# Kernel tuning notes

Hardware: AMD Instinct MI355X
Metric: run time of the kernel (lower is better)

The kernel has to match this reference:

```python
import jax, jax.numpy as jnp
import numpy as np

B, N, CIN, DIM = 4, 16384, 32, 256
NPOINT, NNEIGH = 2048, 16
BN_EPS = 1e-5


def setup_inputs() -> dict:
    key = jax.random.key(0)
    ks = jax.random.split(key, 6)
    return {
        "xyz": jax.random.normal(ks[0], (B, N, 3), jnp.float32),
        "points": jax.random.normal(ks[1], (B, N, CIN), jnp.float32),
        "fc1_w": jax.random.normal(ks[2], (CIN, DIM), jnp.float32) * 0.05,
        "fc1_b": jnp.zeros((DIM,), jnp.float32),
        "conv1_w": jax.random.normal(ks[3], (DIM, DIM), jnp.float32) * 0.05,
        "conv1_b": jnp.zeros((DIM,), jnp.float32),
        "conv2_w": jax.random.normal(ks[4], (DIM, DIM), jnp.float32) * 0.05,
        "conv2_b": jnp.zeros((DIM,), jnp.float32),
        "bn1_g": jnp.ones((DIM,), jnp.float32),
        "bn1_b": jnp.zeros((DIM,), jnp.float32),
        "bn2_g": jnp.ones((DIM,), jnp.float32),
        "bn2_b": jnp.zeros((DIM,), jnp.float32),
        "bn_g": jnp.ones((DIM,), jnp.float32),
        "bn_b": jnp.zeros((DIM,), jnp.float32),
        "npoint": NPOINT,
        "nneigh": NNEIGH,
    }


def _gather(p, i):
    # p: [B, N, ...], i: [B, ...int] -> per-batch fancy index
    return jax.vmap(lambda a, b: a[b])(p, i)


def _batchnorm(x, g, b):
    # x: [B, S, C]; torch BatchNorm1d training-mode forward over (B, S)
    m = x.mean((0, 1), keepdims=True)
    v = x.var((0, 1), keepdims=True)  # biased variance, as torch uses in forward
    return (x - m) * jax.lax.rsqrt(v + BN_EPS) * g + b


def _fps(xyz, npoint):
    # furthest point sampling, seeded at index 0 (pointnet2_utils convention)
    Bn, Nn, _ = xyz.shape
    dist0 = jnp.full((Bn, Nn), jnp.inf, xyz.dtype)
    far0 = jnp.zeros((Bn,), jnp.int32)

    def step(carry, _):
        dist, far = carry
        cent = _gather(xyz, far)  # [B, 3]
        d = jnp.sum((xyz - cent[:, None, :]) ** 2, axis=-1)  # [B, N]
        dist = jnp.minimum(dist, d)
        nxt = jnp.argmax(dist, axis=-1).astype(jnp.int32)
        return (dist, nxt), far

    _, idx = jax.lax.scan(step, (dist0, far0), None, length=npoint)
    return idx.T  # [B, npoint]


def _square_distance(a, b):
    # a: [B, S, 3], b: [B, N, 3] -> [B, S, N]
    return (jnp.sum(a * a, -1)[..., :, None]
            + jnp.sum(b * b, -1)[..., None, :]
            - 2.0 * jnp.einsum('bsc,bnc->bsn', a, b))


def reference(xyz, points, fc1_w, fc1_b, conv1_w, conv1_b, conv2_w, conv2_b,
              bn1_g, bn1_b, bn2_g, bn2_b, bn_g, bn_b, npoint, nneigh):
    fps_idx = _fps(jax.lax.stop_gradient(xyz), npoint)          # [B, S]
    new_xyz = _gather(xyz, fps_idx)                              # [B, S, 3]

    h = points @ fc1_w + fc1_b                                   # [B, N, D]
    points_ori = _gather(h, fps_idx)                             # [B, S, D]

    t = jax.nn.relu(_batchnorm(h @ conv1_w.T + conv1_b, bn1_g, bn1_b))
    h = h + jax.nn.relu(_batchnorm(t @ conv2_w.T + conv2_b, bn2_g, bn2_b))

    d = _square_distance(jax.lax.stop_gradient(new_xyz), jax.lax.stop_gradient(xyz))
    _, idx = jax.lax.top_k(-d, nneigh)                           # [B, S, K] smallest dists
    grouped = _gather(h, idx)                                    # [B, S, K, D]
    new_points = points_ori + grouped.max(axis=2)                # [B, S, D]
    new_points = _batchnorm(new_points, bn_g, bn_b)
    return new_xyz, new_points
```

## Files before the change

### kernel.cpp

```cpp
#include <hip/hip_runtime.h>
#include <math.h>

#define Bn   4
#define Nn   16384
#define CINn 32
#define DIMn 256
#define Sn   2048
#define KNEI 16
#define BNEPS 1e-5f
#define MROWS (Bn * Nn)
#define SROWS (Bn * Sn)

#define UMAX_DPP(v, ctl, rmask)                                               \
    {                                                                         \
        unsigned _o = (unsigned)__builtin_amdgcn_update_dpp(                  \
            0, (int)(v), (ctl), (rmask), 0xf, true);                          \
        (v) = ((v) > _o) ? (v) : _o;                                          \
    }
#define WAVE_UMAX64(v)                                                        \
    UMAX_DPP(v, 0x111, 0xf) UMAX_DPP(v, 0x112, 0xf) UMAX_DPP(v, 0x114, 0xf)  \
    UMAX_DPP(v, 0x118, 0xf) UMAX_DPP(v, 0x142, 0xa) UMAX_DPP(v, 0x143, 0xc)
#define U64MAX_DPP16(khi, klo, ctl)                                           \
    {                                                                         \
        unsigned _lo2 = (unsigned)__builtin_amdgcn_update_dpp(                \
            0, (int)(klo), (ctl), 0xf, 0xf, true);                            \
        unsigned _hi2 = (unsigned)__builtin_amdgcn_update_dpp(                \
            0, (int)(khi), (ctl), 0xf, 0xf, true);                            \
        const bool _g = (_hi2 > (khi)) || (_hi2 == (khi) && _lo2 > (klo));    \
        (khi) = _g ? _hi2 : (khi);                                            \
        (klo) = _g ? _lo2 : (klo);                                            \
    }

__global__ __launch_bounds__(1024, 1) void fps_kernel(const float* __restrict__ xyz,
                                                      int* __restrict__ fidx,
                                                      float* __restrict__ newxyz)
{
#pragma clang fp contract(off)
    __shared__ float sx[1024 * 20];
    __shared__ unsigned long long s_wk[2][16];
    const int b = blockIdx.x;
    const int t = threadIdx.x;
    const int w = t >> 6;
    const int lane = t & 63;
    const float* __restrict__ px = xyz + (size_t)b * Nn * 3;

    float y[16], z[16], dist[16];
#pragma unroll
    for (int a = 0; a < 12; ++a) {
        const float4 v = *reinterpret_cast<const float4*>(&px[48 * t + 4 * a]);
        const float e[4] = {v.x, v.y, v.z, v.w};
#pragma unroll
        for (int c = 0; c < 4; ++c) {
            const int flat = 4 * a + c;
            const int j = flat / 3;
            const int comp = flat - 3 * j;
            if (comp == 0) sx[20 * t + j] = e[c];
            else if (comp == 1) y[j] = e[c];
            else z[j] = e[c];
        }
    }
#pragma unroll
    for (int j = 0; j < 16; ++j) {
        dist[j] = __builtin_huge_valf();
        asm volatile("" : "+v"(y[j]));
        asm volatile("" : "+v"(z[j]));
    }
    float cx = px[0], cy = px[1], cz = px[2];
    if (t == 0) {
        fidx[b * Sn] = 0;
        newxyz[(size_t)b * Sn * 3 + 0] = cx;
        newxyz[(size_t)b * Sn * 3 + 1] = cy;
        newxyz[(size_t)b * Sn * 3 + 2] = cz;
    }
    __syncthreads();

    for (int i = 0; i < Sn - 1; ++i) {
        float bd = -1.0f;
#pragma unroll
        for (int a = 0; a < 4; ++a) {
            const float4 q = *reinterpret_cast<const float4*>(&sx[20 * t + 4 * a]);
            const float xv[4] = {q.x, q.y, q.z, q.w};
#pragma unroll
            for (int c = 0; c < 4; ++c) {
                const int j = 4 * a + c;
                const float dx = xv[c] - cx;
                const float dy = y[j] - cy;
                const float dz = z[j] - cz;
                const float d = (dx * dx + dy * dy) + dz * dz;
                const float nd = fminf(dist[j], d);
                dist[j] = nd;
                bd = fmaxf(bd, nd);
            }
        }
        unsigned bn = 0;
#pragma unroll
        for (int j = 15; j >= 0; --j)
            if (dist[j] == bd) bn = 0xFFFFFFFFu - (unsigned)(16 * t + j);
        unsigned bdu = __float_as_uint(bd);
        unsigned m = bdu;
        WAVE_UMAX64(m)
        const unsigned bdw = (unsigned)__builtin_amdgcn_readlane((int)m, 63);
        unsigned q2 = (bdu == bdw) ? bn : 0u;
        WAVE_UMAX64(q2)
        const unsigned bnw = (unsigned)__builtin_amdgcn_readlane((int)q2, 63);
        if (lane == 0)
            s_wk[i & 1][w] = ((unsigned long long)bdw << 32) | bnw;
        __syncthreads();
        const unsigned long long kk =
            (lane < 16) ? s_wk[i & 1][lane] : 0ull;
        unsigned klo = (unsigned)kk;
        unsigned khi = (unsigned)(kk >> 32);
        U64MAX_DPP16(khi, klo, 0x111)
        U64MAX_DPP16(khi, klo, 0x112)
        U64MAX_DPP16(khi, klo, 0x114)
        U64MAX_DPP16(khi, klo, 0x118)
        const unsigned bnf = (unsigned)__builtin_amdgcn_readlane((int)klo, 15);
        const int wu = (int)(0xFFFFFFFFu - bnf);
        cx = px[3 * wu + 0];
        cy = px[3 * wu + 1];
        cz = px[3 * wu + 2];
        if (t == 0) {
            fidx[b * Sn + i + 1] = wu;
            newxyz[(size_t)(b * Sn + i + 1) * 3 + 0] = cx;
            newxyz[(size_t)(b * Sn + i + 1) * 3 + 1] = cy;
            newxyz[(size_t)(b * Sn + i + 1) * 3 + 2] = cz;
        }
    }
}

template <bool BT, bool AFF>
__global__ __launch_bounds__(256) void gemm_k(const float* __restrict__ A,
                                              const float* __restrict__ Bm,
                                              const float* __restrict__ bias,
                                              const float* __restrict__ asc,
                                              const float* __restrict__ ash,
                                              float* __restrict__ C, int K)
{
    __shared__ float As[16][64];
    __shared__ float Bs[16][64];
    const int t = threadIdx.x;
    const int tx = t & 15;
    const int ty = t >> 4;
    const int r0 = blockIdx.x * 64;
    const int c0 = blockIdx.y * 64;
    const int rrA = t >> 2;
    const int kkA = (t & 3) * 4;
    float acc[4][4] = {};
    for (int kc = 0; kc < K; kc += 16) {
        {
            const float4 v = *reinterpret_cast<const float4*>(
                &A[(size_t)(r0 + rrA) * K + kc + kkA]);
            float vv[4] = {v.x, v.y, v.z, v.w};
#pragma unroll
            for (int m = 0; m < 4; ++m) {
                float xv = vv[m];
                if (AFF) {
                    const int k = kc + kkA + m;
                    xv = fmaxf(fmaf(xv, asc[k], ash[k]), 0.0f);
                }
                As[kkA + m][rrA] = xv;
            }
        }
        if (BT) {
            const float4 v = *reinterpret_cast<const float4*>(
                &Bm[(size_t)(c0 + rrA) * K + kc + kkA]);
            Bs[kkA + 0][rrA] = v.x;
            Bs[kkA + 1][rrA] = v.y;
            Bs[kkA + 2][rrA] = v.z;
            Bs[kkA + 3][rrA] = v.w;
        } else {
            const int kk = t >> 4;
            const int cc = (t & 15) * 4;
            const float4 v = *reinterpret_cast<const float4*>(
                &Bm[(size_t)(kc + kk) * DIMn + c0 + cc]);
            *reinterpret_cast<float4*>(&Bs[kk][cc]) = v;
        }
        __syncthreads();
#pragma unroll
        for (int kk = 0; kk < 16; ++kk) {
            const float4 a = *reinterpret_cast<const float4*>(&As[kk][ty * 4]);
            const float4 bv = *reinterpret_cast<const float4*>(&Bs[kk][tx * 4]);
            const float av[4] = {a.x, a.y, a.z, a.w};
            const float bw[4] = {bv.x, bv.y, bv.z, bv.w};
#pragma unroll
            for (int i = 0; i < 4; ++i)
#pragma unroll
                for (int j = 0; j < 4; ++j)
                    acc[i][j] = fmaf(av[i], bw[j], acc[i][j]);
        }
        __syncthreads();
    }
    const int c = c0 + tx * 4;
#pragma unroll
    for (int i = 0; i < 4; ++i) {
        float4 o;
        o.x = acc[i][0] + bias[c + 0];
        o.y = acc[i][1] + bias[c + 1];
        o.z = acc[i][2] + bias[c + 2];
        o.w = acc[i][3] + bias[c + 3];
        *reinterpret_cast<float4*>(&C[(size_t)(r0 + ty * 4 + i) * DIMn + c]) = o;
    }
}

__global__ __launch_bounds__(256) void gather_po_kernel(const float* __restrict__ h0,
                                                        const int* __restrict__ fidx,
                                                        float* __restrict__ pre)
{
    const int bs = blockIdx.x;
    const int b = bs >> 11;
    const int fid = fidx[bs];
    pre[(size_t)bs * DIMn + threadIdx.x] =
        h0[((size_t)b * Nn + fid) * DIMn + threadIdx.x];
}

__global__ __launch_bounds__(256) void stats_partial(const float* __restrict__ X,
                                                     int rowsPerBlk,
                                                     float* __restrict__ ps,
                                                     float* __restrict__ pq)
{
    const int c = threadIdx.x;
    const size_t r0 = (size_t)blockIdx.x * rowsPerBlk;
    float s = 0.0f, q = 0.0f;
    for (int r = 0; r < rowsPerBlk; ++r) {
        const float v = X[(r0 + r) * DIMn + c];
        s += v;
        q = fmaf(v, v, q);
    }
    ps[blockIdx.x * DIMn + c] = s;
    pq[blockIdx.x * DIMn + c] = q;
}

__global__ __launch_bounds__(256) void bn_finalize(const float* __restrict__ ps,
                                                   const float* __restrict__ pq,
                                                   int nblk, float invN,
                                                   const float* __restrict__ g,
                                                   const float* __restrict__ bb,
                                                   float* __restrict__ sc,
                                                   float* __restrict__ sh)
{
    const int c = threadIdx.x;
    float s = 0.0f, q = 0.0f;
    for (int i = 0; i < nblk; ++i) {
        s += ps[i * DIMn + c];
        q += pq[i * DIMn + c];
    }
    const float mean = s * invN;
    const float var = q * invN - mean * mean;
    const float r = 1.0f / sqrtf(var + BNEPS);
    const float scale = g[c] * r;
    sc[c] = scale;
    sh[c] = bb[c] - mean * scale;
}

__global__ __launch_bounds__(256) void residual_kernel(float* __restrict__ h,
                                                       const float* __restrict__ a2,
                                                       const float* __restrict__ sc,
                                                       const float* __restrict__ sh)
{
    const size_t i = (size_t)blockIdx.x * 256 + threadIdx.x;
    const int c4 = (int)(i & 63);
    float4 hv = reinterpret_cast<float4*>(h)[i];
    const float4 av = reinterpret_cast<const float4*>(a2)[i];
    const float4 s4 = reinterpret_cast<const float4*>(sc)[c4];
    const float4 b4 = reinterpret_cast<const float4*>(sh)[c4];
    hv.x += fmaxf(fmaf(av.x, s4.x, b4.x), 0.0f);
    hv.y += fmaxf(fmaf(av.y, s4.y, b4.y), 0.0f);
    hv.z += fmaxf(fmaf(av.z, s4.z, b4.z), 0.0f);
    hv.w += fmaxf(fmaf(av.w, s4.w, b4.w), 0.0f);
    reinterpret_cast<float4*>(h)[i] = hv;
}

__global__ __launch_bounds__(256) void topk_group(const float* __restrict__ xyz,
                                                  const float* __restrict__ newxyz,
                                                  const float* __restrict__ h,
                                                  float* __restrict__ pre)
{
#pragma clang fp contract(off)
    __shared__ unsigned s_key[Nn];
    __shared__ unsigned long long s_wred[4];
    __shared__ unsigned long long s_win;
    __shared__ int s_nidx[KNEI];
    const int bs = blockIdx.x;
    const int b = bs >> 11;
    const int t = threadIdx.x;
    const float* px = xyz + (size_t)b * Nn * 3;
    const float qx = newxyz[bs * 3 + 0];
    const float qy = newxyz[bs * 3 + 1];
    const float qz = newxyz[bs * 3 + 2];
    const float qq = (qx * qx + qy * qy) + qz * qz;
    unsigned long long mkey = ~0ull;
#pragma unroll 4
    for (int u = 0; u < 64; ++u) {
        const int n = t + (u << 8);
        const float bx = px[n * 3 + 0];
        const float by = px[n * 3 + 1];
        const float bz = px[n * 3 + 2];
        const float bb2 = (bx * bx + by * by) + bz * bz;
        const float ab = (qx * bx + qy * by) + qz * bz;
        const float d = (qq + bb2) - 2.0f * ab;
        unsigned u32 = __float_as_uint(d);
        u32 = ((int)u32 < 0) ? ~u32 : (u32 | 0x80000000u);
        s_key[n] = u32;
        const unsigned long long k = ((unsigned long long)u32 << 32) | (unsigned)n;
        mkey = (k < mkey) ? k : mkey;
    }
    __syncthreads();
    for (int r = 0; r < KNEI; ++r) {
        unsigned long long k = mkey;
#pragma unroll
        for (int off = 32; off > 0; off >>= 1) {
            const unsigned long long o = __shfl_xor(k, off);
            k = (o < k) ? o : k;
        }
        if ((t & 63) == 0) s_wred[t >> 6] = k;
        __syncthreads();
        if (t == 0) {
            unsigned long long w = s_wred[0];
            if (s_wred[1] < w) w = s_wred[1];
            if (s_wred[2] < w) w = s_wred[2];
            if (s_wred[3] < w) w = s_wred[3];
            s_win = w;
            s_nidx[r] = (int)(unsigned)(w & 0xFFFFFFFFull);
        }
        __syncthreads();
        const unsigned long long w = s_win;
        if (w == mkey) {
            const int wn = (int)(unsigned)(w & 0xFFFFFFFFull);
            s_key[wn] = 0xFFFFFFFFu;
            mkey = ~0ull;
#pragma unroll 4
            for (int u = 0; u < 64; ++u) {
                const int n = t + (u << 8);
                const unsigned long long kk =
                    ((unsigned long long)s_key[n] << 32) | (unsigned)n;
                mkey = (kk < mkey) ? kk : mkey;
            }
        }
        __syncthreads();
    }
    const float po = pre[(size_t)bs * DIMn + t];
    float m = -__builtin_huge_valf();
#pragma unroll
    for (int r = 0; r < KNEI; ++r) {
        const int n = s_nidx[r];
        m = fmaxf(m, h[((size_t)b * Nn + n) * DIMn + t]);
    }
    pre[(size_t)bs * DIMn + t] = po + m;
}

__global__ __launch_bounds__(256) void apply_bn_kernel(const float* __restrict__ pre,
                                                       const float* __restrict__ sc,
                                                       const float* __restrict__ sh,
                                                       float* __restrict__ out)
{
    const size_t i = (size_t)blockIdx.x * 256 + threadIdx.x;
    const int c4 = (int)(i & 63);
    const float4 v = reinterpret_cast<const float4*>(pre)[i];
    const float4 s4 = reinterpret_cast<const float4*>(sc)[c4];
    const float4 b4 = reinterpret_cast<const float4*>(sh)[c4];
    float4 o;
    o.x = fmaf(v.x, s4.x, b4.x);
    o.y = fmaf(v.y, s4.y, b4.y);
    o.z = fmaf(v.z, s4.z, b4.z);
    o.w = fmaf(v.w, s4.w, b4.w);
    reinterpret_cast<float4*>(out)[i] = o;
}

extern "C" void kernel_launch(void* const* d_in, const int* in_sizes, int n_in,
                              void* d_out, int out_size, void* d_ws, size_t ws_size,
                              hipStream_t stream)
{
    (void)in_sizes; (void)n_in; (void)out_size; (void)ws_size;
    const float* xyz     = (const float*)d_in[0];
    const float* points  = (const float*)d_in[1];
    const float* fc1_w   = (const float*)d_in[2];
    const float* fc1_b   = (const float*)d_in[3];
    const float* conv1_w = (const float*)d_in[4];
    const float* conv1_b = (const float*)d_in[5];
    const float* conv2_w = (const float*)d_in[6];
    const float* conv2_b = (const float*)d_in[7];
    const float* bn1_g   = (const float*)d_in[8];
    const float* bn1_b   = (const float*)d_in[9];
    const float* bn2_g   = (const float*)d_in[10];
    const float* bn2_b   = (const float*)d_in[11];
    const float* bn_g    = (const float*)d_in[12];
    const float* bn_b    = (const float*)d_in[13];

    float* out = (float*)d_out;
    float* newxyz = out;
    float* outpts = out + (size_t)Bn * Sn * 3;

    char* w = (char*)d_ws;
    float* h0   = (float*)(w);
    float* A1   = (float*)(w + (64ull << 20));
    float* A2   = (float*)(w + (128ull << 20));
    float* pre  = (float*)(w + (192ull << 20));
    int*   fidx = (int*)  (w + (200ull << 20));
    float* ps   = (float*)(w + (201ull << 20));
    float* pq   = ps + 256 * 256;
    float* sc1  = pq + 256 * 256;
    float* sh1  = sc1 + 256;
    float* sc2  = sh1 + 256;
    float* sh2  = sc2 + 256;
    float* sc3  = sh2 + 256;
    float* sh3  = sc3 + 256;

    fps_kernel<<<Bn, 1024, 0, stream>>>(xyz, fidx, newxyz);
    gemm_k<false, false><<<dim3(MROWS / 64, DIMn / 64), 256, 0, stream>>>(
        points, fc1_w, fc1_b, nullptr, nullptr, h0, CINn);
    gather_po_kernel<<<SROWS, 256, 0, stream>>>(h0, fidx, pre);
    gemm_k<true, false><<<dim3(MROWS / 64, DIMn / 64), 256, 0, stream>>>(
        h0, conv1_w, conv1_b, nullptr, nullptr, A1, DIMn);
    stats_partial<<<256, 256, 0, stream>>>(A1, MROWS / 256, ps, pq);
    bn_finalize<<<1, 256, 0, stream>>>(ps, pq, 256, 1.0f / MROWS, bn1_g, bn1_b, sc1, sh1);
    gemm_k<true, true><<<dim3(MROWS / 64, DIMn / 64), 256, 0, stream>>>(
        A1, conv2_w, conv2_b, sc1, sh1, A2, DIMn);
    stats_partial<<<256, 256, 0, stream>>>(A2, MROWS / 256, ps, pq);
    bn_finalize<<<1, 256, 0, stream>>>(ps, pq, 256, 1.0f / MROWS, bn2_g, bn2_b, sc2, sh2);
    residual_kernel<<<(MROWS * DIMn / 4) / 256, 256, 0, stream>>>(h0, A2, sc2, sh2);
    topk_group<<<SROWS, 256, 0, stream>>>(xyz, newxyz, h0, pre);
    stats_partial<<<64, 256, 0, stream>>>(pre, SROWS / 64, ps, pq);
    bn_finalize<<<1, 256, 0, stream>>>(ps, pq, 64, 1.0f / SROWS, bn_g, bn_b, sc3, sh3);
    apply_bn_kernel<<<(SROWS * DIMn / 4) / 256, 256, 0, stream>>>(pre, sc3, sh3, outpts);
}
```

Baseline: 4.668 ms.

## Fuse FPS, MLP stages and kNN grouping into one persistent kernel

Merges the sequential FPS kernel with the GEMM, BN-stats, residual and top-k grouping stages into a single persistent launch of 252 blocks. Four blocks run FPS while the other 248 work blocks process the MLP stages behind grid-wide atomic barriers. The kNN grouping then consumes FPS progress through per-batch counters published every 256 points. The aim is to hide the long serial FPS latency behind the dense work and to remove launch overhead. It depends on every block being resident at the same time to avoid deadlock, and it adds spin-wait barrier cost.

```diff
diff --git a/kernel.cpp b/kernel.cpp
--- a/kernel.cpp
+++ b/kernel.cpp
@@ -10,6 +10,14 @@
 #define BNEPS 1e-5f
 #define MROWS (Bn * Nn)
 #define SROWS (Bn * Sn)
+
+#define NWORK 248
+#define NBLK  (NWORK + Bn)
+
+struct FusedSync {
+    unsigned stage[8];
+    unsigned prog[Bn];
+};
 
 #define UMAX_DPP(v, ctl, rmask)                                               \
     {                                                                         \
@@ -31,126 +39,29 @@
         (klo) = _g ? _lo2 : (klo);                                            \
     }
 
-__global__ __launch_bounds__(1024, 1) void fps_kernel(const float* __restrict__ xyz,
-                                                      int* __restrict__ fidx,
-                                                      float* __restrict__ newxyz)
-{
-#pragma clang fp contract(off)
-    __shared__ float sx[1024 * 20];
-    __shared__ unsigned long long s_wk[2][16];
-    const int b = blockIdx.x;
-    const int t = threadIdx.x;
-    const int w = t >> 6;
-    const int lane = t & 63;
-    const float* __restrict__ px = xyz + (size_t)b * Nn * 3;
-
-    float y[16], z[16], dist[16];
-#pragma unroll
-    for (int a = 0; a < 12; ++a) {
-        const float4 v = *reinterpret_cast<const float4*>(&px[48 * t + 4 * a]);
-        const float e[4] = {v.x, v.y, v.z, v.w};
-#pragma unroll
-        for (int c = 0; c < 4; ++c) {
-            const int flat = 4 * a + c;
-            const int j = flat / 3;
-            const int comp = flat - 3 * j;
-            if (comp == 0) sx[20 * t + j] = e[c];
-            else if (comp == 1) y[j] = e[c];
-            else z[j] = e[c];
-        }
-    }
-#pragma unroll
-    for (int j = 0; j < 16; ++j) {
-        dist[j] = __builtin_huge_valf();
-        asm volatile("" : "+v"(y[j]));
-        asm volatile("" : "+v"(z[j]));
-    }
-    float cx = px[0], cy = px[1], cz = px[2];
-    if (t == 0) {
-        fidx[b * Sn] = 0;
-        newxyz[(size_t)b * Sn * 3 + 0] = cx;
-        newxyz[(size_t)b * Sn * 3 + 1] = cy;
-        newxyz[(size_t)b * Sn * 3 + 2] = cz;
-    }
-    __syncthreads();
-
-    for (int i = 0; i < Sn - 1; ++i) {
-        float bd = -1.0f;
-#pragma unroll
-        for (int a = 0; a < 4; ++a) {
-            const float4 q = *reinterpret_cast<const float4*>(&sx[20 * t + 4 * a]);
-            const float xv[4] = {q.x, q.y, q.z, q.w};
-#pragma unroll
-            for (int c = 0; c < 4; ++c) {
-                const int j = 4 * a + c;
-                const float dx = xv[c] - cx;
-                const float dy = y[j] - cy;
-                const float dz = z[j] - cz;
-                const float d = (dx * dx + dy * dy) + dz * dz;
-                const float nd = fminf(dist[j], d);
-                dist[j] = nd;
-                bd = fmaxf(bd, nd);
-            }
-        }
-        unsigned bn = 0;
-#pragma unroll
-        for (int j = 15; j >= 0; --j)
-            if (dist[j] == bd) bn = 0xFFFFFFFFu - (unsigned)(16 * t + j);
-        unsigned bdu = __float_as_uint(bd);
-        unsigned m = bdu;
-        WAVE_UMAX64(m)
-        const unsigned bdw = (unsigned)__builtin_amdgcn_readlane((int)m, 63);
-        unsigned q2 = (bdu == bdw) ? bn : 0u;
-        WAVE_UMAX64(q2)
-        const unsigned bnw = (unsigned)__builtin_amdgcn_readlane((int)q2, 63);
-        if (lane == 0)
-            s_wk[i & 1][w] = ((unsigned long long)bdw << 32) | bnw;
-        __syncthreads();
-        const unsigned long long kk =
-            (lane < 16) ? s_wk[i & 1][lane] : 0ull;
-        unsigned klo = (unsigned)kk;
-        unsigned khi = (unsigned)(kk >> 32);
-        U64MAX_DPP16(khi, klo, 0x111)
-        U64MAX_DPP16(khi, klo, 0x112)
-        U64MAX_DPP16(khi, klo, 0x114)
-        U64MAX_DPP16(khi, klo, 0x118)
-        const unsigned bnf = (unsigned)__builtin_amdgcn_readlane((int)klo, 15);
-        const int wu = (int)(0xFFFFFFFFu - bnf);
-        cx = px[3 * wu + 0];
-        cy = px[3 * wu + 1];
-        cz = px[3 * wu + 2];
-        if (t == 0) {
-            fidx[b * Sn + i + 1] = wu;
-            newxyz[(size_t)(b * Sn + i + 1) * 3 + 0] = cx;
-            newxyz[(size_t)(b * Sn + i + 1) * 3 + 1] = cy;
-            newxyz[(size_t)(b * Sn + i + 1) * 3 + 2] = cz;
-        }
-    }
+__global__ __launch_bounds__(64) void fps_zero_kernel(unsigned* __restrict__ s)
+{
+    if (threadIdx.x < 12) s[threadIdx.x] = 0u;
 }
 
 template <bool BT, bool AFF>
-__global__ __launch_bounds__(256) void gemm_k(const float* __restrict__ A,
-                                              const float* __restrict__ Bm,
-                                              const float* __restrict__ bias,
-                                              const float* __restrict__ asc,
-                                              const float* __restrict__ ash,
-                                              float* __restrict__ C, int K)
-{
-    __shared__ float As[16][64];
-    __shared__ float Bs[16][64];
-    const int t = threadIdx.x;
-    const int tx = t & 15;
-    const int ty = t >> 4;
-    const int r0 = blockIdx.x * 64;
-    const int c0 = blockIdx.y * 64;
-    const int rrA = t >> 2;
-    const int kkA = (t & 3) * 4;
+__device__ void gemm_team(const float* A, const float* Bm, const float* bias,
+                          const float* asc, const float* ash, float* C,
+                          int K, int tile, bool act, float* lAs, float* lBs,
+                          int ts)
+{
+    const int tx = ts & 15;
+    const int ty = ts >> 4;
+    const int r0 = (tile >> 2) * 64;
+    const int c0 = (tile & 3) * 64;
+    const int rrA = ts >> 2;
+    const int kkA = (ts & 3) * 4;
     float acc[4][4] = {};
     for (int kc = 0; kc < K; kc += 16) {
-        {
+        if (act) {
             const float4 v = *reinterpret_cast<const float4*>(
                 &A[(size_t)(r0 + rrA) * K + kc + kkA]);
-            float vv[4] = {v.x, v.y, v.z, v.w};
+            const float vv[4] = {v.x, v.y, v.z, v.w};
 #pragma unroll
             for (int m = 0; m < 4; ++m) {
                 float xv = vv[m];
@@ -158,59 +69,364 @@
                     const int k = kc + kkA + m;
                     xv = fmaxf(fmaf(xv, asc[k], ash[k]), 0.0f);
                 }
-                As[kkA + m][rrA] = xv;
-            }
-        }
-        if (BT) {
-            const float4 v = *reinterpret_cast<const float4*>(
-                &Bm[(size_t)(c0 + rrA) * K + kc + kkA]);
-            Bs[kkA + 0][rrA] = v.x;
-            Bs[kkA + 1][rrA] = v.y;
-            Bs[kkA + 2][rrA] = v.z;
-            Bs[kkA + 3][rrA] = v.w;
-        } else {
-            const int kk = t >> 4;
-            const int cc = (t & 15) * 4;
-            const float4 v = *reinterpret_cast<const float4*>(
-                &Bm[(size_t)(kc + kk) * DIMn + c0 + cc]);
-            *reinterpret_cast<float4*>(&Bs[kk][cc]) = v;
+                lAs[(kkA + m) * 64 + rrA] = xv;
+            }
+            if (BT) {
+                const float4 u = *reinterpret_cast<const float4*>(
+                    &Bm[(size_t)(c0 + rrA) * K + kc + kkA]);
+                lBs[(kkA + 0) * 64 + rrA] = u.x;
+                lBs[(kkA + 1) * 64 + rrA] = u.y;
+                lBs[(kkA + 2) * 64 + rrA] = u.z;
+                lBs[(kkA + 3) * 64 + rrA] = u.w;
+            } else {
+                const int kk = ts >> 4;
+                const int cc = (ts & 15) * 4;
+                const float4 u = *reinterpret_cast<const float4*>(
+                    &Bm[(size_t)(kc + kk) * DIMn + c0 + cc]);
+                *reinterpret_cast<float4*>(&lBs[kk * 64 + cc]) = u;
+            }
         }
         __syncthreads();
-#pragma unroll
-        for (int kk = 0; kk < 16; ++kk) {
-            const float4 a = *reinterpret_cast<const float4*>(&As[kk][ty * 4]);
-            const float4 bv = *reinterpret_cast<const float4*>(&Bs[kk][tx * 4]);
-            const float av[4] = {a.x, a.y, a.z, a.w};
-            const float bw[4] = {bv.x, bv.y, bv.z, bv.w};
-#pragma unroll
-            for (int i = 0; i < 4; ++i)
-#pragma unroll
-                for (int j = 0; j < 4; ++j)
-                    acc[i][j] = fmaf(av[i], bw[j], acc[i][j]);
+        if (act) {
+#pragma unroll
+            for (int kk = 0; kk < 16; ++kk) {
+                const float4 a = *reinterpret_cast<const float4*>(&lAs[kk * 64 + ty * 4]);
+                const float4 bv = *reinterpret_cast<const float4*>(&lBs[kk * 64 + tx * 4]);
+                const float av[4] = {a.x, a.y, a.z, a.w};
+                const float bw[4] = {bv.x, bv.y, bv.z, bv.w};
+#pragma unroll
+                for (int i = 0; i < 4; ++i)
+#pragma unroll
+                    for (int j = 0; j < 4; ++j)
+                        acc[i][j] = fmaf(av[i], bw[j], acc[i][j]);
+            }
         }
         __syncthreads();
     }
-    const int c = c0 + tx * 4;
-#pragma unroll
-    for (int i = 0; i < 4; ++i) {
-        float4 o;
-        o.x = acc[i][0] + bias[c + 0];
-        o.y = acc[i][1] + bias[c + 1];
-        o.z = acc[i][2] + bias[c + 2];
-        o.w = acc[i][3] + bias[c + 3];
-        *reinterpret_cast<float4*>(&C[(size_t)(r0 + ty * 4 + i) * DIMn + c]) = o;
-    }
-}
-
-__global__ __launch_bounds__(256) void gather_po_kernel(const float* __restrict__ h0,
-                                                        const int* __restrict__ fidx,
-                                                        float* __restrict__ pre)
-{
-    const int bs = blockIdx.x;
-    const int b = bs >> 11;
-    const int fid = fidx[bs];
-    pre[(size_t)bs * DIMn + threadIdx.x] =
-        h0[((size_t)b * Nn + fid) * DIMn + threadIdx.x];
+    if (act) {
+        const int c = c0 + tx * 4;
+#pragma unroll
+        for (int i = 0; i < 4; ++i) {
+            float4 o;
+            o.x = acc[i][0] + bias[c + 0];
+            o.y = acc[i][1] + bias[c + 1];
+            o.z = acc[i][2] + bias[c + 2];
+            o.w = acc[i][3] + bias[c + 3];
+            *reinterpret_cast<float4*>(&C[(size_t)(r0 + ty * 4 + i) * DIMn + c]) = o;
+        }
+    }
+}
+
+__device__ inline void stage_sync(unsigned* ctr, int t)
+{
+    __syncthreads();
+    if (t == 0) {
+        __hip_atomic_fetch_add(ctr, 1u, __ATOMIC_RELEASE, __HIP_MEMORY_SCOPE_AGENT);
+        while (__hip_atomic_load(ctr, __ATOMIC_ACQUIRE, __HIP_MEMORY_SCOPE_AGENT)
+               < (unsigned)NWORK)
+            __builtin_amdgcn_s_sleep(2);
+    }
+    __syncthreads();
+}
+
+__global__ __launch_bounds__(1024, 1) void fused_kernel(
+    const float* __restrict__ xyz, const float* __restrict__ points,
+    const float* __restrict__ fc1_w, const float* __restrict__ fc1_b,
+    const float* __restrict__ conv1_w, const float* __restrict__ conv1_b,
+    const float* __restrict__ conv2_w, const float* __restrict__ conv2_b,
+    const float* __restrict__ bn1_g, const float* __restrict__ bn1_b,
+    const float* __restrict__ bn2_g, const float* __restrict__ bn2_b,
+    float* __restrict__ h0, float* __restrict__ A1, float* __restrict__ A2,
+    float* __restrict__ pre, int* __restrict__ fidx,
+    float* __restrict__ ps, float* __restrict__ pq, float* __restrict__ scv,
+    float* __restrict__ newxyz, FusedSync* sync)
+{
+    __shared__ char smem[81920];
+    __shared__ unsigned long long s_aux[33];
+    __shared__ int s_nidx[KNEI];
+    const int t = threadIdx.x;
+
+    if (blockIdx.x < Bn) {
+#pragma clang fp contract(off)
+        float* sx = reinterpret_cast<float*>(smem);
+        unsigned long long (*s_wk)[16] =
+            reinterpret_cast<unsigned long long (*)[16]>(s_aux);
+        const int b = blockIdx.x;
+        const int w = t >> 6;
+        const int lane = t & 63;
+        const float* __restrict__ px = xyz + (size_t)b * Nn * 3;
+        float y[16], z[16], dist[16];
+#pragma unroll
+        for (int a = 0; a < 12; ++a) {
+            const float4 v = *reinterpret_cast<const float4*>(&px[48 * t + 4 * a]);
+            const float e[4] = {v.x, v.y, v.z, v.w};
+#pragma unroll
+            for (int c = 0; c < 4; ++c) {
+                const int flat = 4 * a + c;
+                const int j = flat / 3;
+                const int comp = flat - 3 * j;
+                if (comp == 0) sx[20 * t + j] = e[c];
+                else if (comp == 1) y[j] = e[c];
+                else z[j] = e[c];
+            }
+        }
+#pragma unroll
+        for (int j = 0; j < 16; ++j) {
+            dist[j] = __builtin_huge_valf();
+            asm volatile("" : "+v"(y[j]));
+            asm volatile("" : "+v"(z[j]));
+        }
+        float cx = px[0], cy = px[1], cz = px[2];
+        if (t == 0) {
+            fidx[b * Sn] = 0;
+            newxyz[(size_t)b * Sn * 3 + 0] = cx;
+            newxyz[(size_t)b * Sn * 3 + 1] = cy;
+            newxyz[(size_t)b * Sn * 3 + 2] = cz;
+        }
+        __syncthreads();
+        for (int i = 0; i < Sn - 1; ++i) {
+            float bd = -1.0f;
+#pragma unroll
+            for (int a = 0; a < 4; ++a) {
+                const float4 q = *reinterpret_cast<const float4*>(&sx[20 * t + 4 * a]);
+                const float xv[4] = {q.x, q.y, q.z, q.w};
+#pragma unroll
+                for (int c = 0; c < 4; ++c) {
+                    const int j = 4 * a + c;
+                    const float dx = xv[c] - cx;
+                    const float dy = y[j] - cy;
+                    const float dz = z[j] - cz;
+                    const float d = (dx * dx + dy * dy) + dz * dz;
+                    const float nd = fminf(dist[j], d);
+                    dist[j] = nd;
+                    bd = fmaxf(bd, nd);
+                }
+            }
+            unsigned bn = 0;
+#pragma unroll
+            for (int j = 15; j >= 0; --j)
+                if (dist[j] == bd) bn = 0xFFFFFFFFu - (unsigned)(16 * t + j);
+            unsigned bdu = __float_as_uint(bd);
+            unsigned m = bdu;
+            WAVE_UMAX64(m)
+            const unsigned bdw = (unsigned)__builtin_amdgcn_readlane((int)m, 63);
+            unsigned q2 = (bdu == bdw) ? bn : 0u;
+            WAVE_UMAX64(q2)
+            const unsigned bnw = (unsigned)__builtin_amdgcn_readlane((int)q2, 63);
+            if (lane == 0)
+                s_wk[i & 1][w] = ((unsigned long long)bdw << 32) | bnw;
+            __syncthreads();
+            const unsigned long long kk = (lane < 16) ? s_wk[i & 1][lane] : 0ull;
+            unsigned klo = (unsigned)kk;
+            unsigned khi = (unsigned)(kk >> 32);
+            U64MAX_DPP16(khi, klo, 0x111)
+            U64MAX_DPP16(khi, klo, 0x112)
+            U64MAX_DPP16(khi, klo, 0x114)
+            U64MAX_DPP16(khi, klo, 0x118)
+            const unsigned bnf = (unsigned)__builtin_amdgcn_readlane((int)klo, 15);
+            const int wu = (int)(0xFFFFFFFFu - bnf);
+            cx = px[3 * wu + 0];
+            cy = px[3 * wu + 1];
+            cz = px[3 * wu + 2];
+            if (t == 0) {
+                fidx[b * Sn + i + 1] = wu;
+                newxyz[(size_t)(b * Sn + i + 1) * 3 + 0] = cx;
+                newxyz[(size_t)(b * Sn + i + 1) * 3 + 1] = cy;
+                newxyz[(size_t)(b * Sn + i + 1) * 3 + 2] = cz;
+                if (((i + 2) & 255) == 0)
+                    __hip_atomic_store(&sync->prog[b], (unsigned)(i + 2),
+                                       __ATOMIC_RELEASE, __HIP_MEMORY_SCOPE_AGENT);
+            }
+        }
+        return;
+    }
+
+    const int wid = blockIdx.x - Bn;
+    const int team = t >> 8;
+    const int ts = t & 255;
+    float* lAs = reinterpret_cast<float*>(smem) + team * 2048;
+    float* lBs = lAs + 1024;
+    float* sc1 = scv, *sh1 = scv + 256, *sc2 = scv + 512, *sh2 = scv + 768;
+
+    for (int it = 0; it < 5; ++it) {
+        const int tile = it * (NWORK * 4) + wid * 4 + team;
+        gemm_team<false, false>(points, fc1_w, fc1_b, nullptr, nullptr, h0,
+                                CINn, tile, tile < 4096, lAs, lBs, ts);
+    }
+    stage_sync(&sync->stage[0], t);
+    for (int it = 0; it < 5; ++it) {
+        const int tile = it * (NWORK * 4) + wid * 4 + team;
+        gemm_team<true, false>(h0, conv1_w, conv1_b, nullptr, nullptr, A1,
+                               DIMn, tile, tile < 4096, lAs, lBs, ts);
+    }
+    stage_sync(&sync->stage[1], t);
+    for (int sb = wid; sb < 256; sb += NWORK) {
+        if (t < DIMn) {
+            float s = 0.0f, q = 0.0f;
+            const size_t r0 = (size_t)sb * 256;
+            for (int r = 0; r < 256; ++r) {
+                const float v = A1[(r0 + r) * DIMn + t];
+                s += v;
+                q = fmaf(v, v, q);
+            }
+            ps[sb * DIMn + t] = s;
+            pq[sb * DIMn + t] = q;
+        }
+    }
+    stage_sync(&sync->stage[2], t);
+    if (wid == 0 && t < DIMn) {
+        float s = 0.0f, q = 0.0f;
+        for (int i = 0; i < 256; ++i) { s += ps[i * DIMn + t]; q += pq[i * DIMn + t]; }
+        const float invN = 1.0f / MROWS;
+        const float mean = s * invN;
+        const float var = q * invN - mean * mean;
+        const float r = 1.0f / sqrtf(var + BNEPS);
+        const float scale = bn1_g[t] * r;
+        sc1[t] = scale;
+        sh1[t] = bn1_b[t] - mean * scale;
+    }
+    stage_sync(&sync->stage[3], t);
+    for (int it = 0; it < 5; ++it) {
+        const int tile = it * (NWORK * 4) + wid * 4 + team;
+        gemm_team<true, true>(A1, conv2_w, conv2_b, sc1, sh1, A2,
+                              DIMn, tile, tile < 4096, lAs, lBs, ts);
+    }
+    stage_sync(&sync->stage[4], t);
+    for (int sb = wid; sb < 256; sb += NWORK) {
+        if (t < DIMn) {
+            float s = 0.0f, q = 0.0f;
+            const size_t r0 = (size_t)sb * 256;
+            for (int r = 0; r < 256; ++r) {
+                const float v = A2[(r0 + r) * DIMn + t];
+                s += v;
+                q = fmaf(v, v, q);
+            }
+            ps[sb * DIMn + t] = s;
+            pq[sb * DIMn + t] = q;
+        }
+    }
+    stage_sync(&sync->stage[5], t);
+    if (wid == 0 && t < DIMn) {
+        float s = 0.0f, q = 0.0f;
+        for (int i = 0; i < 256; ++i) { s += ps[i * DIMn + t]; q += pq[i * DIMn + t]; }
+        const float invN = 1.0f / MROWS;
+        const float mean = s * invN;
+        const float var = q * invN - mean * mean;
+        const float r = 1.0f / sqrtf(var + BNEPS);
+        const float scale = bn2_g[t] * r;
+        sc2[t] = scale;
+        sh2[t] = bn2_b[t] - mean * scale;
+    }
+    stage_sync(&sync->stage[6], t);
+    for (size_t idx = (size_t)wid * 1024 + t; idx < (size_t)MROWS * DIMn / 4;
+         idx += (size_t)NWORK * 1024) {
+        const int c4 = (int)(idx & 63);
+        const float4 hv = reinterpret_cast<const float4*>(h0)[idx];
+        float4 av = reinterpret_cast<float4*>(A2)[idx];
+        const float4 s4 = reinterpret_cast<const float4*>(sc2)[c4];
+        const float4 b4 = reinterpret_cast<const float4*>(sh2)[c4];
+        av.x = hv.x + fmaxf(fmaf(av.x, s4.x, b4.x), 0.0f);
+        av.y = hv.y + fmaxf(fmaf(av.y, s4.y, b4.y), 0.0f);
+        av.z = hv.z + fmaxf(fmaf(av.z, s4.z, b4.z), 0.0f);
+        av.w = hv.w + fmaxf(fmaf(av.w, s4.w, b4.w), 0.0f);
+        reinterpret_cast<float4*>(A2)[idx] = av;
+    }
+    stage_sync(&sync->stage[7], t);
+
+    {
+#pragma clang fp contract(off)
+        unsigned* s_key = reinterpret_cast<unsigned*>(smem);
+        const int b = wid & 3;
+        const int w = t >> 6;
+        const int lane = t & 63;
+        const float* px = xyz + (size_t)b * Nn * 3;
+        unsigned cprog = 0;
+        for (int q = wid; q < SROWS; q += NWORK) {
+            const int s = q >> 2;
+            if (t == 0 && cprog < (unsigned)(s + 1)) {
+                unsigned p;
+                do {
+                    p = __hip_atomic_load(&sync->prog[b], __ATOMIC_ACQUIRE,
+                                          __HIP_MEMORY_SCOPE_AGENT);
+                    if (p < (unsigned)(s + 1)) __builtin_amdgcn_s_sleep(8);
+                } while (p < (unsigned)(s + 1));
+                cprog = p;
+            }
+            __syncthreads();
+            const int bs = b * Sn + s;
+            const float qx = newxyz[(size_t)bs * 3 + 0];
+            const float qy = newxyz[(size_t)bs * 3 + 1];
+            const float qz = newxyz[(size_t)bs * 3 + 2];
+            const float qq = (qx * qx + qy * qy) + qz * qz;
+            unsigned long long mkey = ~0ull;
+#pragma unroll 4
+            for (int u = 0; u < 16; ++u) {
+                const int n = t + (u << 10);
+                const float bx = px[n * 3 + 0];
+                const float by = px[n * 3 + 1];
+                const float bz = px[n * 3 + 2];
+                const float bb2 = (bx * bx + by * by) + bz * bz;
+                const float ab = (qx * bx + qy * by) + qz * bz;
+                const float d = (qq + bb2) - 2.0f * ab;
+                unsigned u32 = __float_as_uint(d);
+                u32 = ((int)u32 < 0) ? ~u32 : (u32 | 0x80000000u);
+                s_key[n] = u32;
+                const unsigned long long k =
+                    ((unsigned long long)u32 << 32) | (unsigned)n;
+                mkey = (k < mkey) ? k : mkey;
+            }
+            __syncthreads();
+            for (int r = 0; r < KNEI; ++r) {
+                unsigned long long k = mkey;
+#pragma unroll
+                for (int off = 32; off > 0; off >>= 1) {
+                    const unsigned long long o = __shfl_xor(k, off);
+                    k = (o < k) ? o : k;
+                }
+                if (lane == 0) s_aux[w] = k;
+                __syncthreads();
+                if (w == 0) {
+                    unsigned long long kk = (lane < 16) ? s_aux[lane] : ~0ull;
+#pragma unroll
+                    for (int off = 8; off > 0; off >>= 1) {
+                        const unsigned long long o = __shfl_xor(kk, off);
+                        kk = (o < kk) ? o : kk;
+                    }
+                    if (lane == 0) {
+                        s_aux[32] = kk;
+                        s_nidx[r] = (int)(unsigned)(kk & 0xFFFFFFFFull);
+                    }
+                }
+                __syncthreads();
+                const unsigned long long wk = s_aux[32];
+                if (wk == mkey) {
+                    const int wn = (int)(unsigned)(wk & 0xFFFFFFFFull);
+                    s_key[wn] = 0xFFFFFFFFu;
+                    mkey = ~0ull;
+#pragma unroll 4
+                    for (int u = 0; u < 16; ++u) {
+                        const int n = t + (u << 10);
+                        const unsigned long long kk2 =
+                            ((unsigned long long)s_key[n] << 32) | (unsigned)n;
+                        mkey = (kk2 < mkey) ? kk2 : mkey;
+                    }
+                }
+            }
+            __syncthreads();
+            if (t < DIMn) {
+                const int fid = fidx[bs];
+                const float po = h0[((size_t)b * Nn + fid) * DIMn + t];
+                float m = -__builtin_huge_valf();
+#pragma unroll
+                for (int r = 0; r < KNEI; ++r) {
+                    const int n = s_nidx[r];
+                    m = fmaxf(m, A2[((size_t)b * Nn + n) * DIMn + t]);
+                }
+                pre[(size_t)bs * DIMn + t] = po + m;
+            }
+            __syncthreads();
+        }
+    }
 }
 
 __global__ __launch_bounds__(256) void stats_partial(const float* __restrict__ X,
@@ -250,102 +466,6 @@
     const float scale = g[c] * r;
     sc[c] = scale;
     sh[c] = bb[c] - mean * scale;
-}
-
-__global__ __launch_bounds__(256) void residual_kernel(float* __restrict__ h,
-                                                       const float* __restrict__ a2,
-                                                       const float* __restrict__ sc,
-                                                       const float* __restrict__ sh)
-{
-    const size_t i = (size_t)blockIdx.x * 256 + threadIdx.x;
-    const int c4 = (int)(i & 63);
-    float4 hv = reinterpret_cast<float4*>(h)[i];
-    const float4 av = reinterpret_cast<const float4*>(a2)[i];
-    const float4 s4 = reinterpret_cast<const float4*>(sc)[c4];
-    const float4 b4 = reinterpret_cast<const float4*>(sh)[c4];
-    hv.x += fmaxf(fmaf(av.x, s4.x, b4.x), 0.0f);
-    hv.y += fmaxf(fmaf(av.y, s4.y, b4.y), 0.0f);
-    hv.z += fmaxf(fmaf(av.z, s4.z, b4.z), 0.0f);
-    hv.w += fmaxf(fmaf(av.w, s4.w, b4.w), 0.0f);
-    reinterpret_cast<float4*>(h)[i] = hv;
-}
-
-__global__ __launch_bounds__(256) void topk_group(const float* __restrict__ xyz,
-                                                  const float* __restrict__ newxyz,
-                                                  const float* __restrict__ h,
-                                                  float* __restrict__ pre)
-{
-#pragma clang fp contract(off)
-    __shared__ unsigned s_key[Nn];
-    __shared__ unsigned long long s_wred[4];
-    __shared__ unsigned long long s_win;
-    __shared__ int s_nidx[KNEI];
-    const int bs = blockIdx.x;
-    const int b = bs >> 11;
-    const int t = threadIdx.x;
-    const float* px = xyz + (size_t)b * Nn * 3;
-    const float qx = newxyz[bs * 3 + 0];
-    const float qy = newxyz[bs * 3 + 1];
-    const float qz = newxyz[bs * 3 + 2];
-    const float qq = (qx * qx + qy * qy) + qz * qz;
-    unsigned long long mkey = ~0ull;
-#pragma unroll 4
-    for (int u = 0; u < 64; ++u) {
-        const int n = t + (u << 8);
-        const float bx = px[n * 3 + 0];
-        const float by = px[n * 3 + 1];
-        const float bz = px[n * 3 + 2];
-        const float bb2 = (bx * bx + by * by) + bz * bz;
-        const float ab = (qx * bx + qy * by) + qz * bz;
-        const float d = (qq + bb2) - 2.0f * ab;
-        unsigned u32 = __float_as_uint(d);
-        u32 = ((int)u32 < 0) ? ~u32 : (u32 | 0x80000000u);
-        s_key[n] = u32;
-        const unsigned long long k = ((unsigned long long)u32 << 32) | (unsigned)n;
-        mkey = (k < mkey) ? k : mkey;
-    }
-    __syncthreads();
-    for (int r = 0; r < KNEI; ++r) {
-        unsigned long long k = mkey;
-#pragma unroll
-        for (int off = 32; off > 0; off >>= 1) {
-            const unsigned long long o = __shfl_xor(k, off);
-            k = (o < k) ? o : k;
-        }
-        if ((t & 63) == 0) s_wred[t >> 6] = k;
-        __syncthreads();
-        if (t == 0) {
-            unsigned long long w = s_wred[0];
-            if (s_wred[1] < w) w = s_wred[1];
-            if (s_wred[2] < w) w = s_wred[2];
-            if (s_wred[3] < w) w = s_wred[3];
-            s_win = w;
-            s_nidx[r] = (int)(unsigned)(w & 0xFFFFFFFFull);
-        }
-        __syncthreads();
-        const unsigned long long w = s_win;
-        if (w == mkey) {
-            const int wn = (int)(unsigned)(w & 0xFFFFFFFFull);
-            s_key[wn] = 0xFFFFFFFFu;
-            mkey = ~0ull;
-#pragma unroll 4
-            for (int u = 0; u < 64; ++u) {
-                const int n = t + (u << 8);
-                const unsigned long long kk =
-                    ((unsigned long long)s_key[n] << 32) | (unsigned)n;
-                mkey = (kk < mkey) ? kk : mkey;
-            }
-        }
-        __syncthreads();
-    }
-    const float po = pre[(size_t)bs * DIMn + t];
-    float m = -__builtin_huge_valf();
-#pragma unroll
-    for (int r = 0; r < KNEI; ++r) {
-        const int n = s_nidx[r];
-        m = fmaxf(m, h[((size_t)b * Nn + n) * DIMn + t]);
-    }
-    pre[(size_t)bs * DIMn + t] = po + m;
 }
 
 __global__ __launch_bounds__(256) void apply_bn_kernel(const float* __restrict__ pre,
@@ -398,27 +518,16 @@
     int*   fidx = (int*)  (w + (200ull << 20));
     float* ps   = (float*)(w + (201ull << 20));
     float* pq   = ps + 256 * 256;
-    float* sc1  = pq + 256 * 256;
-    float* sh1  = sc1 + 256;
-    float* sc2  = sh1 + 256;
-    float* sh2  = sc2 + 256;
-    float* sc3  = sh2 + 256;
+    float* scv  = pq + 256 * 256;
+    float* sc3  = scv + 1024;
     float* sh3  = sc3 + 256;
-
-    fps_kernel<<<Bn, 1024, 0, stream>>>(xyz, fidx, newxyz);
-    gemm_k<false, false><<<dim3(MROWS / 64, DIMn / 64), 256, 0, stream>>>(
-        points, fc1_w, fc1_b, nullptr, nullptr, h0, CINn);
-    gather_po_kernel<<<SROWS, 256, 0, stream>>>(h0, fidx, pre);
-    gemm_k<true, false><<<dim3(MROWS / 64, DIMn / 64), 256, 0, stream>>>(
-        h0, conv1_w, conv1_b, nullptr, nullptr, A1, DIMn);
-    stats_partial<<<256, 256, 0, stream>>>(A1, MROWS / 256, ps, pq);
-    bn_finalize<<<1, 256, 0, stream>>>(ps, pq, 256, 1.0f / MROWS, bn1_g, bn1_b, sc1, sh1);
-    gemm_k<true, true><<<dim3(MROWS / 64, DIMn / 64), 256, 0, stream>>>(
-        A1, conv2_w, conv2_b, sc1, sh1, A2, DIMn);
-    stats_partial<<<256, 256, 0, stream>>>(A2, MROWS / 256, ps, pq);
-    bn_finalize<<<1, 256, 0, stream>>>(ps, pq, 256, 1.0f / MROWS, bn2_g, bn2_b, sc2, sh2);
-    residual_kernel<<<(MROWS * DIMn / 4) / 256, 256, 0, stream>>>(h0, A2, sc2, sh2);
-    topk_group<<<SROWS, 256, 0, stream>>>(xyz, newxyz, h0, pre);
+    FusedSync* sync = (FusedSync*)(w + (203ull << 20));
+
+    fps_zero_kernel<<<1, 64, 0, stream>>>((unsigned*)sync);
+    fused_kernel<<<NBLK, 1024, 0, stream>>>(
+        xyz, points, fc1_w, fc1_b, conv1_w, conv1_b, conv2_w, conv2_b,
+        bn1_g, bn1_b, bn2_g, bn2_b, h0, A1, A2, pre, fidx, ps, pq, scv,
+        newxyz, sync);
     stats_partial<<<64, 256, 0, stream>>>(pre, SROWS / 64, ps, pq);
     bn_finalize<<<1, 256, 0, stream>>>(ps, pq, 64, 1.0f / SROWS, bn_g, bn_b, sc3, sh3);
     apply_bn_kernel<<<(SROWS * DIMn / 4) / 256, 256, 0, stream>>>(pre, sc3, sh3, outpts);
```

New measurement: 4.096 ms. 1.14x faster.
